# Optimization experiments

Hardware: AMD Instinct MI355X
Metric: run time of the kernel (lower is better)

Reference implementation:

```python
import jax, jax.numpy as jnp
import numpy as np

N, E, B = 25000, 400000, 64          # nodes, edges, graphs
F, ED, H, C = 32, 8, 4, 32           # feature/edge dims, heads, per-head dim
HC = H * C
L = 4                                # init conv + 3 stacked convs (same shapes)
LIN = 128


def setup_inputs() -> dict:
    key = jax.random.key(0)
    ks = jax.random.split(key, 24)
    s = 0.05
    inp = {
        "x": jax.random.normal(ks[0], (N, F), jnp.float32),
        "edge_attr": jax.random.normal(ks[1], (E, ED), jnp.float32),
        "edge_index": jax.random.randint(ks[2], (2, E), 0, N),
        "batch_index": jnp.sort(jax.random.randint(ks[3], (N,), 0, B)),
        # stacked TransformerConv params (leading dim = layer)
        "Wq": jax.random.normal(ks[4], (L, F, HC), jnp.float32) * s,
        "bq": jnp.zeros((L, HC), jnp.float32),
        "Wk": jax.random.normal(ks[5], (L, F, HC), jnp.float32) * s,
        "bk": jnp.zeros((L, HC), jnp.float32),
        "Wv": jax.random.normal(ks[6], (L, F, HC), jnp.float32) * s,
        "bv": jnp.zeros((L, HC), jnp.float32),
        "We": jax.random.normal(ks[7], (L, ED, HC), jnp.float32) * s,
        "be": jnp.zeros((L, HC), jnp.float32),
        "Wskip": jax.random.normal(ks[8], (L, F, HC), jnp.float32) * s,
        "bskip": jnp.zeros((L, HC), jnp.float32),
        "Wbeta": jax.random.normal(ks[9], (L, 3 * HC, 1), jnp.float32) * s,
        # per-layer Linear(H*C -> emb) + BatchNorm
        "Wlin": jax.random.normal(ks[10], (L, HC, F), jnp.float32) * s,
        "blin": jnp.zeros((L, F), jnp.float32),
        "bn_gamma": jnp.ones((L, F), jnp.float32),
        "bn_beta": jnp.zeros((L, F), jnp.float32),
        # readout MLP
        "W1": jax.random.normal(ks[11], (2 * F, LIN), jnp.float32) * s,
        "b1": jnp.zeros((LIN,), jnp.float32),
        "W2": jax.random.normal(ks[12], (LIN, LIN // 2), jnp.float32) * s,
        "b2": jnp.zeros((LIN // 2,), jnp.float32),
        "W3": jax.random.normal(ks[13], (LIN // 2, 1), jnp.float32) * s,
        "b3": jnp.zeros((1,), jnp.float32),
    }
    return inp


def _transformer_conv(x, edge_attr, src, dst, Wq, bq, Wk, bk, Wv, bv, We, be,
                      Wskip, bskip, Wbeta):
    """PyG TransformerConv(heads=H, concat=True, beta=True, edge_dim=ED), eval mode."""
    n = x.shape[0]
    q = (x @ Wq + bq).reshape(n, H, C)
    k = (x @ Wk + bk).reshape(n, H, C)
    v = (x @ Wv + bv).reshape(n, H, C)
    e = (edge_attr @ We + be).reshape(-1, H, C)          # [E,H,C]
    kj = k[src] + e                                       # key_j + edge
    alpha = jnp.einsum('ehc,ehc->eh', q[dst], kj) / np.sqrt(C).astype(np.float32)
    # segment softmax over incoming edges per destination node
    amax = jax.ops.segment_max(alpha, dst, num_segments=n)
    a = jnp.exp(alpha - amax[dst])
    denom = jax.ops.segment_sum(a, dst, num_segments=n)
    a = a / denom[dst]                                    # [E,H]
    msg = (v[src] + e) * a[:, :, None]
    out = jax.ops.segment_sum(msg, dst, num_segments=n).reshape(n, HC)
    x_skip = x @ Wskip + bskip
    beta = jax.nn.sigmoid(
        jnp.concatenate([out, x_skip, out - x_skip], axis=-1) @ Wbeta)  # [N,1]
    return beta * x_skip + (1.0 - beta) * out


def _bn(h, gamma, beta):
    m = h.mean(axis=0)
    v = h.var(axis=0)
    return (h - m) * jax.lax.rsqrt(v + 1e-5) * gamma + beta


def reference(x, edge_attr, edge_index, batch_index,
              Wq, bq, Wk, bk, Wv, bv, We, be, Wskip, bskip, Wbeta,
              Wlin, blin, bn_gamma, bn_beta, W1, b1, W2, b2, W3, b3):
    src, dst = edge_index[0], edge_index[1]
    counts = jax.ops.segment_sum(jnp.ones((N,), jnp.float32), batch_index,
                                 num_segments=B)[:, None]
    h = x
    rep = jnp.zeros((B, 2 * F), jnp.float32)
    for i in range(L):
        h = _transformer_conv(h, edge_attr, src, dst,
                              Wq[i], bq[i], Wk[i], bk[i], Wv[i], bv[i],
                              We[i], be[i], Wskip[i], bskip[i], Wbeta[i])
        h = jax.nn.elu(h @ Wlin[i] + blin[i])
        h = _bn(h, bn_gamma[i], bn_beta[i])
        if i > 0:  # original pools only inside the n_layers loop
            gmx = jax.ops.segment_max(h, batch_index, num_segments=B)
            gmean = jax.ops.segment_sum(h, batch_index, num_segments=B) / counts
            rep = rep + jnp.concatenate([gmx, gmean], axis=1)
    z = jax.nn.elu(rep @ W1 + b1)
    z = jax.nn.elu(z @ W2 + b2)
    return z @ W3 + b3  # [B,1]
```

## Files before the change

### kernel.cpp

```cpp
#include <hip/hip_runtime.h>
#include <hip/hip_bf16.h>
#include <hip/hip_fp16.h>
#include <math.h>

#define NN 25000
#define EE 400000
#define BB 64
#define FF 32
#define EDD 8
#define HH 4
#define CC 32
#define HCC 128
#define LL 4
#define LINN 128

#define RSQRT_C 0.17677669529663687f
#define NREP 16
#define LSTATS_WORDS (NREP * 64)


__global__ void deg_kernel(const int* __restrict__ dst, int* __restrict__ deg) {
    int i = blockIdx.x * blockDim.x + threadIdx.x;
    if (i < EE) atomicAdd(&deg[dst[i]], 1);
}

__global__ void gstart_kernel(const int* __restrict__ bidx, int* __restrict__ gstart) {
    int b = threadIdx.x;
    if (b <= BB) {
        int lo = 0, hi = NN;
        while (lo < hi) { int mid = (lo + hi) >> 1; if (bidx[mid] < b) lo = mid + 1; else hi = mid; }
        gstart[b] = lo;
    }
}

__global__ void scan1_kernel(const int* __restrict__ deg, int* __restrict__ rowp, int* __restrict__ blks) {
    __shared__ int s[256];
    int i = blockIdx.x * 256 + threadIdx.x;
    int v = (i < NN) ? deg[i] : 0;
    s[threadIdx.x] = v;
    __syncthreads();
    for (int off = 1; off < 256; off <<= 1) {
        int t = (threadIdx.x >= off) ? s[threadIdx.x - off] : 0;
        __syncthreads();
        s[threadIdx.x] += t;
        __syncthreads();
    }
    if (i < NN) rowp[i + 1] = s[threadIdx.x];
    if (threadIdx.x == 255) blks[blockIdx.x] = s[255];
    if (i == 0) rowp[0] = 0;
}

__global__ void scan2_kernel(int* __restrict__ blks, int nb) {
    __shared__ int s[128];
    int t = threadIdx.x;
    int v = (t < nb) ? blks[t] : 0;
    s[t] = v;
    __syncthreads();
    for (int off = 1; off < 128; off <<= 1) {
        int u = (t >= off) ? s[t - off] : 0;
        __syncthreads();
        s[t] += u;
        __syncthreads();
    }
    if (t < nb) blks[t] = s[t] - v;
}

__global__ void scan3_kernel(int* __restrict__ rowp, const int* __restrict__ blks) {
    int i = blockIdx.x * 256 + threadIdx.x;
    if (i < NN) rowp[i + 1] += blks[blockIdx.x];
}

__global__ void fill_kernel(const int* __restrict__ dst, const int* __restrict__ rowp,
                            int* __restrict__ cnt2, int* __restrict__ eid) {
    int i = blockIdx.x * blockDim.x + threadIdx.x;
    if (i < EE) {
        int d = dst[i];
        int pos = rowp[d] + atomicAdd(&cnt2[d], 1);
        eid[pos] = i;
    }
}

__global__ void sortseg_kernel(const int* __restrict__ rowp, int* __restrict__ eid) {
    int n = blockIdx.x * 256 + threadIdx.x;
    if (n >= NN) return;
    int b = rowp[n], e = rowp[n + 1];
    int d = e - b;
    if (d <= 1) return;
    if (d <= 64) {
        int buf[64];
        for (int i = 0; i < d; ++i) buf[i] = eid[b + i];
        for (int i = 1; i < d; ++i) {
            int key = buf[i];
            int j = i - 1;
            while (j >= 0 && buf[j] > key) { buf[j + 1] = buf[j]; --j; }
            buf[j + 1] = key;
        }
        for (int i = 0; i < d; ++i) eid[b + i] = buf[i];
    } else {
        for (int i = b + 1; i < e; ++i) {
            int key = eid[i];
            int j = i - 1;
            while (j >= b && eid[j] > key) { eid[j + 1] = eid[j]; --j; }
            eid[j + 1] = key;
        }
    }
}

__global__ void csr_gather_kernel(const int* __restrict__ csre, const int* __restrict__ srcA,
                                  const float* __restrict__ eattr,
                                  int* __restrict__ csrsrc, float4* __restrict__ ecsr) {
    int j = blockIdx.x * blockDim.x + threadIdx.x;
    if (j < EE) {
        int e = csre[j];
        csrsrc[j] = srcA[e];
        const float4* s = (const float4*)(eattr + (size_t)e * 8);
        ecsr[(size_t)j * 2] = s[0];
        ecsr[(size_t)j * 2 + 1] = s[1];
    }
}

__global__ __launch_bounds__(256) void qkvs_kernel(
    const float* __restrict__ hin,
    const float* __restrict__ Wq, const float* __restrict__ bq,
    const float* __restrict__ Wk, const float* __restrict__ bk,
    const float* __restrict__ Wv, const float* __restrict__ bv,
    const float* __restrict__ Ws, const float* __restrict__ bs,
    float2* __restrict__ qo,
    __half2* __restrict__ kvo,
    float2* __restrict__ so, float* __restrict__ lstats)
{
    if (blockIdx.x == 0) {
        for (int i = threadIdx.x; i < LSTATS_WORDS; i += 256) lstats[i] = 0.0f;
    }
    __shared__ float xs[32][32];
    int lane = threadIdx.x & 63;
    int sel = threadIdx.x >> 6;
    const float* W = (sel == 0) ? Wq : (sel == 1) ? Wk : (sel == 2) ? Wv : Ws;
    const float* bias = (sel == 0) ? bq : (sel == 1) ? bk : (sel == 2) ? bv : bs;
    float w0[32], w1[32];
#pragma unroll
    for (int f = 0; f < 32; ++f) {
        float2 t = *(const float2*)&W[f * 128 + 2 * lane];
        w0[f] = t.x; w1[f] = t.y;
    }
    float2 bvv = *(const float2*)&bias[2 * lane];

    int c = lane >> 1;
    int pr = lane & 1;
    int f2idx = c * 2 + pr;
    int h2k   = c * 4 + pr;
    int h2v   = c * 4 + 2 + pr;

    for (int chunk = blockIdx.x * 32; chunk < NN; chunk += gridDim.x * 32) {
        __syncthreads();
        for (int i = threadIdx.x; i < 1024; i += 256) {
            int nn = chunk + (i >> 5);
            xs[i >> 5][i & 31] = (nn < NN) ? hin[nn * 32 + (i & 31)] : 0.0f;
        }
        __syncthreads();
        int nmax = NN - chunk; if (nmax > 32) nmax = 32;
        for (int nl = 0; nl < nmax; ++nl) {
            float a0 = bvv.x, a1 = bvv.y;
#pragma unroll
            for (int f = 0; f < 32; ++f) {
                float xv = xs[nl][f];
                a0 += xv * w0[f];
                a1 += xv * w1[f];
            }
            size_t node = (size_t)(chunk + nl);
            if (sel == 0)      qo[node * 64 + f2idx] = make_float2(a0, a1);
            else if (sel == 1) kvo[node * 128 + h2k] = __float22half2_rn(make_float2(a0, a1));
            else if (sel == 2) kvo[node * 128 + h2v] = __float22half2_rn(make_float2(a0, a1));
            else               so[node * 64 + f2idx] = make_float2(a0, a1);
        }
    }
}

__global__ __launch_bounds__(256) void attn_kernel(
    const float4* __restrict__ qb4, const uint4* __restrict__ kvb4,
    const float4* __restrict__ skb4,
    const float4* __restrict__ eb4,
    const int* __restrict__ srcArr,
    const int* __restrict__ rowp,
    const float* __restrict__ WeL, const float* __restrict__ beL,
    const float* __restrict__ WbL,
    const float* __restrict__ WlinL, const float* __restrict__ blinL,
    float* __restrict__ hlin, float* __restrict__ bnpart)
{
    __shared__ __align__(16) float shc[4 * 128];
    __shared__ float sbn[64];

    int tid = threadIdx.x;
    if (tid < 64) sbn[tid] = 0.0f;
    __syncthreads();

    int w = tid >> 6;
    int lane = tid & 63;
    int n = blockIdx.x * 4 + w;

    if (n < NN) {
        int c = lane & 31;
        int h = lane >> 5;

        float4 q4 = qb4[(size_t)n * 32 + c];
        q4.x *= RSQRT_C; q4.y *= RSQRT_C; q4.z *= RSQRT_C; q4.w *= RSQRT_C;

        float r[8];
        float qbe;
        {
#pragma unroll
            for (int d = 0; d < 8; ++d) {
                float4 wd = *(const float4*)&WeL[d * 128 + 4 * c];
                r[d] = q4.x * wd.x + q4.y * wd.y + q4.z * wd.z + q4.w * wd.w;
            }
            float4 be4 = *(const float4*)&beL[4 * c];
            qbe = q4.x * be4.x + q4.y * be4.y + q4.z * be4.z + q4.w * be4.w;
#pragma unroll
            for (int off = 1; off <= 4; off <<= 1) {
#pragma unroll
                for (int d = 0; d < 8; ++d) r[d] += __shfl_xor(r[d], off);
                qbe += __shfl_xor(qbe, off);
            }
        }

        int beg = rowp[n], end = rowp[n + 1];
        int cnt = end - beg;
        int last = end - 1;

        float s = 0.0f, a0 = 0.0f, a1 = 0.0f, a2 = 0.0f, a3 = 0.0f;
        float t0 = 0.f, t1 = 0.f, t2 = 0.f, t3 = 0.f, t4 = 0.f, t5 = 0.f, t6 = 0.f, t7 = 0.f;

        uint4 kvA = make_uint4(0u, 0u, 0u, 0u), kvB = kvA;
        float4 eaA0 = make_float4(0.f, 0.f, 0.f, 0.f), eaA1 = eaA0;
        float4 eaB0 = eaA0, eaB1 = eaA0;
        int snC = 0, snD = 0;

        if (cnt > 0) {
            int j0 = beg + h;     j0 = (j0 < end) ? j0 : last;
            int j1 = beg + 2 + h; j1 = (j1 < end) ? j1 : last;
            int j2 = beg + 4 + h; j2 = (j2 < end) ? j2 : last;
            int j3 = beg + 6 + h; j3 = (j3 < end) ? j3 : last;
            int snA = srcArr[j0];
            int snB = srcArr[j1];
            snC = srcArr[j2];
            snD = srcArr[j3];
            kvA  = kvb4[(size_t)snA * 32 + c];
            kvB  = kvb4[(size_t)snB * 32 + c];
            eaA0 = eb4[(size_t)j0 * 2];
            eaA1 = eb4[(size_t)j0 * 2 + 1];
            eaB0 = eb4[(size_t)j1 * 2];
            eaB1 = eb4[(size_t)j1 * 2 + 1];
        }

        for (int jb = beg; jb < end; jb += 2) {
            int j = jb + h;
            uint4 kvC = kvb4[(size_t)snC * 32 + c];
            int jn = (j + 4 < end) ? j + 4 : last;
            float4 eaC0 = eb4[(size_t)jn * 2];
            float4 eaC1 = eb4[(size_t)jn * 2 + 1];
            int j8 = (j + 8 < end) ? j + 8 : last;
            int snE = srcArr[j8];

            float2 k01 = __half22float2(*(const __half2*)&kvA.x);
            float2 k23 = __half22float2(*(const __half2*)&kvA.y);
            float2 v01 = __half22float2(*(const __half2*)&kvA.z);
            float2 v23 = __half22float2(*(const __half2*)&kvA.w);

            float p = q4.x * k01.x + q4.y * k01.y + q4.z * k23.x + q4.w * k23.y;
            p += __shfl_xor(p, 1);
            p += __shfl_xor(p, 2);
            p += __shfl_xor(p, 4);
            float pe = eaA0.x * r[0] + eaA0.y * r[1] + eaA0.z * r[2] + eaA0.w * r[3]
                     + eaA1.x * r[4] + eaA1.y * r[5] + eaA1.z * r[6] + eaA1.w * r[7] + qbe;
            float wg = (j < end) ? __expf(p + pe) : 0.0f;
            s += wg;
            a0 = fmaf(wg, v01.x, a0);
            a1 = fmaf(wg, v01.y, a1);
            a2 = fmaf(wg, v23.x, a2);
            a3 = fmaf(wg, v23.y, a3);
            t0 = fmaf(wg, eaA0.x, t0);
            t1 = fmaf(wg, eaA0.y, t1);
            t2 = fmaf(wg, eaA0.z, t2);
            t3 = fmaf(wg, eaA0.w, t3);
            t4 = fmaf(wg, eaA1.x, t4);
            t5 = fmaf(wg, eaA1.y, t5);
            t6 = fmaf(wg, eaA1.z, t6);
            t7 = fmaf(wg, eaA1.w, t7);

            kvA = kvB; kvB = kvC;
            eaA0 = eaB0; eaA1 = eaB1; eaB0 = eaC0; eaB1 = eaC1;
            snC = snD; snD = snE;
        }

        s  += __shfl_xor(s, 32);
        a0 += __shfl_xor(a0, 32);
        a1 += __shfl_xor(a1, 32);
        a2 += __shfl_xor(a2, 32);
        a3 += __shfl_xor(a3, 32);
        t0 += __shfl_xor(t0, 32);
        t1 += __shfl_xor(t1, 32);
        t2 += __shfl_xor(t2, 32);
        t3 += __shfl_xor(t3, 32);
        t4 += __shfl_xor(t4, 32);
        t5 += __shfl_xor(t5, 32);
        t6 += __shfl_xor(t6, 32);
        t7 += __shfl_xor(t7, 32);

        {
            float4 wd;
            wd = *(const float4*)&WeL[0 * 128 + 4 * c];
            a0 = fmaf(t0, wd.x, a0); a1 = fmaf(t0, wd.y, a1); a2 = fmaf(t0, wd.z, a2); a3 = fmaf(t0, wd.w, a3);
            wd = *(const float4*)&WeL[1 * 128 + 4 * c];
            a0 = fmaf(t1, wd.x, a0); a1 = fmaf(t1, wd.y, a1); a2 = fmaf(t1, wd.z, a2); a3 = fmaf(t1, wd.w, a3);
            wd = *(const float4*)&WeL[2 * 128 + 4 * c];
            a0 = fmaf(t2, wd.x, a0); a1 = fmaf(t2, wd.y, a1); a2 = fmaf(t2, wd.z, a2); a3 = fmaf(t2, wd.w, a3);
            wd = *(const float4*)&WeL[3 * 128 + 4 * c];
            a0 = fmaf(t3, wd.x, a0); a1 = fmaf(t3, wd.y, a1); a2 = fmaf(t3, wd.z, a2); a3 = fmaf(t3, wd.w, a3);
            wd = *(const float4*)&WeL[4 * 128 + 4 * c];
            a0 = fmaf(t4, wd.x, a0); a1 = fmaf(t4, wd.y, a1); a2 = fmaf(t4, wd.z, a2); a3 = fmaf(t4, wd.w, a3);
            wd = *(const float4*)&WeL[5 * 128 + 4 * c];
            a0 = fmaf(t5, wd.x, a0); a1 = fmaf(t5, wd.y, a1); a2 = fmaf(t5, wd.z, a2); a3 = fmaf(t5, wd.w, a3);
            wd = *(const float4*)&WeL[6 * 128 + 4 * c];
            a0 = fmaf(t6, wd.x, a0); a1 = fmaf(t6, wd.y, a1); a2 = fmaf(t6, wd.z, a2); a3 = fmaf(t6, wd.w, a3);
            wd = *(const float4*)&WeL[7 * 128 + 4 * c];
            a0 = fmaf(t7, wd.x, a0); a1 = fmaf(t7, wd.y, a1); a2 = fmaf(t7, wd.z, a2); a3 = fmaf(t7, wd.w, a3);
            float4 be4 = *(const float4*)&beL[4 * c];
            a0 = fmaf(s, be4.x, a0);
            a1 = fmaf(s, be4.y, a1);
            a2 = fmaf(s, be4.z, a2);
            a3 = fmaf(s, be4.w, a3);
        }

        float rs = (cnt > 0) ? (1.0f / s) : 0.0f;
        float o0 = a0 * rs, o1 = a1 * rs, o2 = a2 * rs, o3 = a3 * rs;

        float4 sk4 = skb4[(size_t)n * 32 + c];
        float4 wbo = *(const float4*)&WbL[4 * c];
        float4 wbs = *(const float4*)&WbL[128 + 4 * c];
        float4 wbd = *(const float4*)&WbL[256 + 4 * c];

        float t = o0 * wbo.x + sk4.x * wbs.x + (o0 - sk4.x) * wbd.x
                + o1 * wbo.y + sk4.y * wbs.y + (o1 - sk4.y) * wbd.y
                + o2 * wbo.z + sk4.z * wbs.z + (o2 - sk4.z) * wbd.z
                + o3 * wbo.w + sk4.w * wbs.w + (o3 - sk4.w) * wbd.w;
#pragma unroll
        for (int off = 1; off <= 16; off <<= 1) t += __shfl_xor(t, off);
        float beta = 1.0f / (1.0f + __expf(-t));
        float4 hc4;
        hc4.x = beta * sk4.x + (1.0f - beta) * o0;
        hc4.y = beta * sk4.y + (1.0f - beta) * o1;
        hc4.z = beta * sk4.z + (1.0f - beta) * o2;
        hc4.w = beta * sk4.w + (1.0f - beta) * o3;
        if (h == 0) ((float4*)shc)[w * 32 + c] = hc4;
        int cc = lane & 31;
        int half = lane >> 5;
        float acc = 0.0f;
#pragma unroll 8
        for (int i = 0; i < 64; ++i) {
            int ch = half * 64 + i;
            acc += shc[w * 128 + ch] * WlinL[ch * 32 + cc];
        }
        acc += __shfl_xor(acc, 32);
        if (lane < 32) {
            float hv = acc + blinL[lane];
            hv = (hv > 0.0f) ? hv : expm1f(hv);
            hlin[n * 32 + lane] = hv;
            atomicAdd(&sbn[lane], hv);
            atomicAdd(&sbn[32 + lane], hv * hv);
        }
    }
    __syncthreads();
    if (tid < 64) atomicAdd(&bnpart[(blockIdx.x & (NREP - 1)) * 64 + tid], sbn[tid]);
}

__global__ __launch_bounds__(256) void bnpool_kernel(
    const float* __restrict__ hlin, const float* __restrict__ bnpart,
    const float* __restrict__ gamma, const float* __restrict__ bnbeta,
    const int* __restrict__ gstart,
    float* __restrict__ hc, float* __restrict__ rep, int doPool)
{
    __shared__ float sscale[32], sshift[32];
    __shared__ float smax[8][32], ssum[8][32];
    int tid = threadIdx.x;
    int ch = tid & 31, row = tid >> 5;
    if (tid < 32) {
        float sm = 0.0f, sq = 0.0f;
#pragma unroll
        for (int r = 0; r < NREP; ++r) { sm += bnpart[r * 64 + tid]; sq += bnpart[r * 64 + 32 + tid]; }
        float mean = sm * (1.0f / NN);
        float var = sq * (1.0f / NN) - mean * mean;
        float scale = gamma[tid] * rsqrtf(var + 1e-5f);
        sscale[tid] = scale;
        sshift[tid] = bnbeta[tid] - mean * scale;
    }
    __syncthreads();
    int g = blockIdx.x;
    int gs = gstart[g], ge = gstart[g + 1];
    float scale = sscale[ch], shift = sshift[ch];
    float mx = -1e30f, sum = 0.0f;
    for (int n = gs + row; n < ge; n += 8) {
        float val = hlin[n * 32 + ch] * scale + shift;
        hc[n * 32 + ch] = val;
        mx = fmaxf(mx, val);
        sum += val;
    }
    if (doPool) {
        smax[row][ch] = mx; ssum[row][ch] = sum;
        __syncthreads();
        if (row == 0) {
#pragma unroll
            for (int r = 1; r < 8; ++r) { mx = fmaxf(mx, smax[r][ch]); sum += ssum[r][ch]; }
            int cntg = ge - gs;
            if (cntg > 0) {
                rep[g * 64 + ch]      += mx;
                rep[g * 64 + 32 + ch] += sum / (float)cntg;
            }
        }
    }
}

__device__ __forceinline__ float eluf(float x) { return x > 0.0f ? x : expm1f(x); }

__global__ __launch_bounds__(128) void readout_kernel(
    const float* __restrict__ rep,
    const float* __restrict__ W1, const float* __restrict__ b1,
    const float* __restrict__ W2, const float* __restrict__ b2,
    const float* __restrict__ W3, const float* __restrict__ b3,
    float* __restrict__ out)
{
    __shared__ float sr[64];
    __shared__ float sz1[128];
    __shared__ float sz2[64];
    int g = blockIdx.x;
    int t = threadIdx.x;
    if (t < 64) sr[t] = rep[g * 64 + t];
    __syncthreads();
    float acc = b1[t];
#pragma unroll 8
    for (int i = 0; i < 64; ++i) acc += sr[i] * W1[i * 128 + t];
    sz1[t] = eluf(acc);
    __syncthreads();
    if (t < 64) {
        float a2 = b2[t];
#pragma unroll 8
        for (int i = 0; i < 128; ++i) a2 += sz1[i] * W2[i * 64 + t];
        sz2[t] = eluf(a2);
    }
    __syncthreads();
    if (t < 64) {
        float p = sz2[t] * W3[t];
#pragma unroll
        for (int off = 1; off <= 32; off <<= 1) p += __shfl_xor(p, off);
        if (t == 0) out[g] = p + b3[0];
    }
}


extern "C" void kernel_launch(void* const* d_in, const int* in_sizes, int n_in,
                              void* d_out, int out_size, void* d_ws, size_t ws_size,
                              hipStream_t stream) {
    const float* x      = (const float*)d_in[0];
    const float* eattr  = (const float*)d_in[1];
    const int*   eidx   = (const int*)d_in[2];
    const int*   bidx   = (const int*)d_in[3];
    const float* Wq     = (const float*)d_in[4];
    const float* bq     = (const float*)d_in[5];
    const float* Wk     = (const float*)d_in[6];
    const float* bk     = (const float*)d_in[7];
    const float* Wv     = (const float*)d_in[8];
    const float* bv     = (const float*)d_in[9];
    const float* We     = (const float*)d_in[10];
    const float* be     = (const float*)d_in[11];
    const float* Wskip  = (const float*)d_in[12];
    const float* bskip  = (const float*)d_in[13];
    const float* Wbeta  = (const float*)d_in[14];
    const float* Wlin   = (const float*)d_in[15];
    const float* blin   = (const float*)d_in[16];
    const float* bng    = (const float*)d_in[17];
    const float* bnb    = (const float*)d_in[18];
    const float* W1     = (const float*)d_in[19];
    const float* b1     = (const float*)d_in[20];
    const float* W2     = (const float*)d_in[21];
    const float* b2     = (const float*)d_in[22];
    const float* W3     = (const float*)d_in[23];
    const float* b3     = (const float*)d_in[24];
    float* out = (float*)d_out;

    char* ws = (char*)d_ws;
    size_t off = 0;
    auto alloc = [&](size_t bytes) -> char* {
        char* p = ws + off;
        off = (off + bytes + 255) & ~(size_t)255;
        return p;
    };
    int*    rowp   = (int*)alloc((NN + 1) * 4);
    int*    degcnt = (int*)alloc(2 * NN * 4);
    int*    deg    = degcnt;
    int*    cnt2   = degcnt + NN;
    int*    csre   = (int*)alloc(EE * 4);
    int*    blks   = (int*)alloc(128 * 4);
    int*    gstart = (int*)alloc((BB + 1) * 4);
    float*  rep    = (float*)alloc(BB * 64 * 4);
    float4* qB     = (float4*)alloc((size_t)NN * 32 * 16);
    uint4*  kvB    = (uint4*)alloc((size_t)NN * 32 * 16);
    float4* skB    = (float4*)alloc((size_t)NN * 32 * 16);
    float*  hlin   = (float*)alloc((size_t)NN * 32 * 4);
    float*  hcur   = (float*)alloc((size_t)NN * 32 * 4);
    float*  bnpart = (float*)alloc(LSTATS_WORDS * 4);
    int*    csrsrc = (int*)alloc(EE * 4);
    float4* ecsr   = (float4*)alloc((size_t)EE * 32);

    const int* srcA = eidx;
    const int* dstA = eidx + EE;

    (void)hipMemsetAsync(degcnt, 0, 2 * NN * 4, stream);
    (void)hipMemsetAsync(rep, 0, BB * 64 * 4, stream);

    deg_kernel<<<(EE + 255) / 256, 256, 0, stream>>>(dstA, deg);
    gstart_kernel<<<1, 128, 0, stream>>>(bidx, gstart);
    scan1_kernel<<<98, 256, 0, stream>>>(deg, rowp, blks);
    scan2_kernel<<<1, 128, 0, stream>>>(blks, 98);
    scan3_kernel<<<98, 256, 0, stream>>>(rowp, blks);
    fill_kernel<<<(EE + 255) / 256, 256, 0, stream>>>(dstA, rowp, cnt2, csre);
    sortseg_kernel<<<98, 256, 0, stream>>>(rowp, csre);
    csr_gather_kernel<<<(EE + 255) / 256, 256, 0, stream>>>(csre, srcA, eattr, csrsrc, ecsr);

    const float* hin = x;
    for (int l = 0; l < LL; ++l) {
        qkvs_kernel<<<782, 256, 0, stream>>>(
            hin,
            Wq + l * FF * HCC, bq + l * HCC,
            Wk + l * FF * HCC, bk + l * HCC,
            Wv + l * FF * HCC, bv + l * HCC,
            Wskip + l * FF * HCC, bskip + l * HCC,
            (float2*)qB, (__half2*)kvB, (float2*)skB, bnpart);

        attn_kernel<<<(NN + 3) / 4, 256, 0, stream>>>(
            qB, kvB, skB, ecsr, csrsrc, rowp,
            We + l * EDD * HCC, be + l * HCC,
            Wbeta + l * 3 * HCC,
            Wlin + l * HCC * FF, blin + l * FF,
            hlin, bnpart);

        bnpool_kernel<<<BB, 256, 0, stream>>>(hlin, bnpart, bng + l * FF, bnb + l * FF,
                                              gstart, hcur, rep, (l > 0) ? 1 : 0);
        hin = hcur;
    }

    readout_kernel<<<64, 128, 0, stream>>>(rep, W1, b1, W2, b2, W3, b3, out);
}
```

Baseline: 590.0 us.

## Split K/V into separate arrays and process four edges per wave

```diff
diff --git a/kernel.cpp b/kernel.cpp
--- a/kernel.cpp
+++ b/kernel.cpp
@@ -125,9 +125,9 @@
     const float* __restrict__ Wk, const float* __restrict__ bk,
     const float* __restrict__ Wv, const float* __restrict__ bv,
     const float* __restrict__ Ws, const float* __restrict__ bs,
-    float2* __restrict__ qo,
-    __half2* __restrict__ kvo,
-    float2* __restrict__ so, float* __restrict__ lstats)
+    float2* __restrict__ qo, __half2* __restrict__ ko,
+    __half2* __restrict__ vo, float2* __restrict__ so,
+    float* __restrict__ lstats)
 {
     if (blockIdx.x == 0) {
         for (int i = threadIdx.x; i < LSTATS_WORDS; i += 256) lstats[i] = 0.0f;
@@ -145,12 +145,6 @@
     }
     float2 bvv = *(const float2*)&bias[2 * lane];
 
-    int c = lane >> 1;
-    int pr = lane & 1;
-    int f2idx = c * 2 + pr;
-    int h2k   = c * 4 + pr;
-    int h2v   = c * 4 + 2 + pr;
-
     for (int chunk = blockIdx.x * 32; chunk < NN; chunk += gridDim.x * 32) {
         __syncthreads();
         for (int i = threadIdx.x; i < 1024; i += 256) {
@@ -168,17 +162,17 @@
                 a1 += xv * w1[f];
             }
             size_t node = (size_t)(chunk + nl);
-            if (sel == 0)      qo[node * 64 + f2idx] = make_float2(a0, a1);
-            else if (sel == 1) kvo[node * 128 + h2k] = __float22half2_rn(make_float2(a0, a1));
-            else if (sel == 2) kvo[node * 128 + h2v] = __float22half2_rn(make_float2(a0, a1));
-            else               so[node * 64 + f2idx] = make_float2(a0, a1);
+            if (sel == 0)      qo[node * 64 + lane] = make_float2(a0, a1);
+            else if (sel == 1) ko[node * 64 + lane] = __float22half2_rn(make_float2(a0, a1));
+            else if (sel == 2) vo[node * 64 + lane] = __float22half2_rn(make_float2(a0, a1));
+            else               so[node * 64 + lane] = make_float2(a0, a1);
         }
     }
 }
 
 __global__ __launch_bounds__(256) void attn_kernel(
-    const float4* __restrict__ qb4, const uint4* __restrict__ kvb4,
-    const float4* __restrict__ skb4,
+    const float4* __restrict__ qb4, const uint4* __restrict__ kb4,
+    const uint4* __restrict__ vb4, const float4* __restrict__ skb4,
     const float4* __restrict__ eb4,
     const int* __restrict__ srcArr,
     const int* __restrict__ rowp,
@@ -199,24 +193,30 @@
     int n = blockIdx.x * 4 + w;
 
     if (n < NN) {
-        int c = lane & 31;
-        int h = lane >> 5;
-
-        float4 q4 = qb4[(size_t)n * 32 + c];
-        q4.x *= RSQRT_C; q4.y *= RSQRT_C; q4.z *= RSQRT_C; q4.w *= RSQRT_C;
+        int cl = lane & 15;
+        int qt = lane >> 4;
+
+        const float4* qp = qb4 + (size_t)n * 32 + cl * 2;
+        float4 qa = qp[0], qb = qp[1];
+        qa.x *= RSQRT_C; qa.y *= RSQRT_C; qa.z *= RSQRT_C; qa.w *= RSQRT_C;
+        qb.x *= RSQRT_C; qb.y *= RSQRT_C; qb.z *= RSQRT_C; qb.w *= RSQRT_C;
 
         float r[8];
         float qbe;
         {
 #pragma unroll
             for (int d = 0; d < 8; ++d) {
-                float4 wd = *(const float4*)&WeL[d * 128 + 4 * c];
-                r[d] = q4.x * wd.x + q4.y * wd.y + q4.z * wd.z + q4.w * wd.w;
+                float4 wa = *(const float4*)&WeL[d * 128 + 8 * cl];
+                float4 wb = *(const float4*)&WeL[d * 128 + 8 * cl + 4];
+                r[d] = qa.x * wa.x + qa.y * wa.y + qa.z * wa.z + qa.w * wa.w
+                     + qb.x * wb.x + qb.y * wb.y + qb.z * wb.z + qb.w * wb.w;
             }
-            float4 be4 = *(const float4*)&beL[4 * c];
-            qbe = q4.x * be4.x + q4.y * be4.y + q4.z * be4.z + q4.w * be4.w;
-#pragma unroll
-            for (int off = 1; off <= 4; off <<= 1) {
+            float4 bea = *(const float4*)&beL[8 * cl];
+            float4 beb = *(const float4*)&beL[8 * cl + 4];
+            qbe = qa.x * bea.x + qa.y * bea.y + qa.z * bea.z + qa.w * bea.w
+                + qb.x * beb.x + qb.y * beb.y + qb.z * beb.z + qb.w * beb.w;
+#pragma unroll
+            for (int off = 1; off <= 2; off <<= 1) {
 #pragma unroll
                 for (int d = 0; d < 8; ++d) r[d] += __shfl_xor(r[d], off);
                 qbe += __shfl_xor(qbe, off);
@@ -227,57 +227,69 @@
         int cnt = end - beg;
         int last = end - 1;
 
-        float s = 0.0f, a0 = 0.0f, a1 = 0.0f, a2 = 0.0f, a3 = 0.0f;
+        float s = 0.0f;
+        float a0 = 0.f, a1 = 0.f, a2 = 0.f, a3 = 0.f, a4 = 0.f, a5 = 0.f, a6 = 0.f, a7 = 0.f;
         float t0 = 0.f, t1 = 0.f, t2 = 0.f, t3 = 0.f, t4 = 0.f, t5 = 0.f, t6 = 0.f, t7 = 0.f;
 
-        uint4 kvA = make_uint4(0u, 0u, 0u, 0u), kvB = kvA;
-        float4 eaA0 = make_float4(0.f, 0.f, 0.f, 0.f), eaA1 = eaA0;
-        float4 eaB0 = eaA0, eaB1 = eaA0;
+        uint4 kA = make_uint4(0u,0u,0u,0u), vA = kA, kB = kA, vB = kA;
+        float4 eaA0 = make_float4(0.f,0.f,0.f,0.f), eaA1 = eaA0, eaB0 = eaA0, eaB1 = eaA0;
         int snC = 0, snD = 0;
 
         if (cnt > 0) {
-            int j0 = beg + h;     j0 = (j0 < end) ? j0 : last;
-            int j1 = beg + 2 + h; j1 = (j1 < end) ? j1 : last;
-            int j2 = beg + 4 + h; j2 = (j2 < end) ? j2 : last;
-            int j3 = beg + 6 + h; j3 = (j3 < end) ? j3 : last;
+            int j0 = beg + qt;      j0 = (j0 < end) ? j0 : last;
+            int j1 = beg + 4 + qt;  j1 = (j1 < end) ? j1 : last;
+            int j2 = beg + 8 + qt;  j2 = (j2 < end) ? j2 : last;
+            int j3 = beg + 12 + qt; j3 = (j3 < end) ? j3 : last;
             int snA = srcArr[j0];
             int snB = srcArr[j1];
             snC = srcArr[j2];
             snD = srcArr[j3];
-            kvA  = kvb4[(size_t)snA * 32 + c];
-            kvB  = kvb4[(size_t)snB * 32 + c];
+            kA = kb4[(size_t)snA * 16 + cl];
+            vA = vb4[(size_t)snA * 16 + cl];
+            kB = kb4[(size_t)snB * 16 + cl];
+            vB = vb4[(size_t)snB * 16 + cl];
             eaA0 = eb4[(size_t)j0 * 2];
             eaA1 = eb4[(size_t)j0 * 2 + 1];
             eaB0 = eb4[(size_t)j1 * 2];
             eaB1 = eb4[(size_t)j1 * 2 + 1];
         }
 
-        for (int jb = beg; jb < end; jb += 2) {
-            int j = jb + h;
-            uint4 kvC = kvb4[(size_t)snC * 32 + c];
-            int jn = (j + 4 < end) ? j + 4 : last;
+        for (int jb = beg; jb < end; jb += 4) {
+            int j = jb + qt;
+            uint4 kC = kb4[(size_t)snC * 16 + cl];
+            uint4 vC = vb4[(size_t)snC * 16 + cl];
+            int jn = (j + 8 < end) ? j + 8 : last;
             float4 eaC0 = eb4[(size_t)jn * 2];
             float4 eaC1 = eb4[(size_t)jn * 2 + 1];
-            int j8 = (j + 8 < end) ? j + 8 : last;
-            int snE = srcArr[j8];
-
-            float2 k01 = __half22float2(*(const __half2*)&kvA.x);
-            float2 k23 = __half22float2(*(const __half2*)&kvA.y);
-            float2 v01 = __half22float2(*(const __half2*)&kvA.z);
-            float2 v23 = __half22float2(*(const __half2*)&kvA.w);
-
-            float p = q4.x * k01.x + q4.y * k01.y + q4.z * k23.x + q4.w * k23.y;
+            int j16 = (j + 16 < end) ? j + 16 : last;
+            int snE = srcArr[j16];
+
+            float2 k01 = __half22float2(*(const __half2*)&kA.x);
+            float2 k23 = __half22float2(*(const __half2*)&kA.y);
+            float2 k45 = __half22float2(*(const __half2*)&kA.z);
+            float2 k67 = __half22float2(*(const __half2*)&kA.w);
+
+            float p = qa.x * k01.x + qa.y * k01.y + qa.z * k23.x + qa.w * k23.y
+                    + qb.x * k45.x + qb.y * k45.y + qb.z * k67.x + qb.w * k67.y;
             p += __shfl_xor(p, 1);
             p += __shfl_xor(p, 2);
-            p += __shfl_xor(p, 4);
             float pe = eaA0.x * r[0] + eaA0.y * r[1] + eaA0.z * r[2] + eaA0.w * r[3]
                      + eaA1.x * r[4] + eaA1.y * r[5] + eaA1.z * r[6] + eaA1.w * r[7] + qbe;
             float wg = (j < end) ? __expf(p + pe) : 0.0f;
             s += wg;
+
+            float2 v01 = __half22float2(*(const __half2*)&vA.x);
+            float2 v23 = __half22float2(*(const __half2*)&vA.y);
+            float2 v45 = __half22float2(*(const __half2*)&vA.z);
+            float2 v67 = __half22float2(*(const __half2*)&vA.w);
             a0 = fmaf(wg, v01.x, a0);
             a1 = fmaf(wg, v01.y, a1);
             a2 = fmaf(wg, v23.x, a2);
             a3 = fmaf(wg, v23.y, a3);
+            a4 = fmaf(wg, v45.x, a4);
+            a5 = fmaf(wg, v45.y, a5);
+            a6 = fmaf(wg, v67.x, a6);
+            a7 = fmaf(wg, v67.y, a7);
             t0 = fmaf(wg, eaA0.x, t0);
             t1 = fmaf(wg, eaA0.y, t1);
             t2 = fmaf(wg, eaA0.z, t2);
@@ -287,71 +299,81 @@
             t6 = fmaf(wg, eaA1.z, t6);
             t7 = fmaf(wg, eaA1.w, t7);
 
-            kvA = kvB; kvB = kvC;
+            kA = kB; vA = vB; kB = kC; vB = vC;
             eaA0 = eaB0; eaA1 = eaB1; eaB0 = eaC0; eaB1 = eaC1;
             snC = snD; snD = snE;
         }
 
-        s  += __shfl_xor(s, 32);
-        a0 += __shfl_xor(a0, 32);
-        a1 += __shfl_xor(a1, 32);
-        a2 += __shfl_xor(a2, 32);
-        a3 += __shfl_xor(a3, 32);
-        t0 += __shfl_xor(t0, 32);
-        t1 += __shfl_xor(t1, 32);
-        t2 += __shfl_xor(t2, 32);
-        t3 += __shfl_xor(t3, 32);
-        t4 += __shfl_xor(t4, 32);
-        t5 += __shfl_xor(t5, 32);
-        t6 += __shfl_xor(t6, 32);
-        t7 += __shfl_xor(t7, 32);
+#pragma unroll
+        for (int off = 16; off <= 32; off <<= 1) {
+            s  += __shfl_xor(s, off);
+            a0 += __shfl_xor(a0, off); a1 += __shfl_xor(a1, off);
+            a2 += __shfl_xor(a2, off); a3 += __shfl_xor(a3, off);
+            a4 += __shfl_xor(a4, off); a5 += __shfl_xor(a5, off);
+            a6 += __shfl_xor(a6, off); a7 += __shfl_xor(a7, off);
+            t0 += __shfl_xor(t0, off); t1 += __shfl_xor(t1, off);
+            t2 += __shfl_xor(t2, off); t3 += __shfl_xor(t3, off);
+            t4 += __shfl_xor(t4, off); t5 += __shfl_xor(t5, off);
+            t6 += __shfl_xor(t6, off); t7 += __shfl_xor(t7, off);
+        }
 
         {
-            float4 wd;
-            wd = *(const float4*)&WeL[0 * 128 + 4 * c];
-            a0 = fmaf(t0, wd.x, a0); a1 = fmaf(t0, wd.y, a1); a2 = fmaf(t0, wd.z, a2); a3 = fmaf(t0, wd.w, a3);
-            wd = *(const float4*)&WeL[1 * 128 + 4 * c];
-            a0 = fmaf(t1, wd.x, a0); a1 = fmaf(t1, wd.y, a1); a2 = fmaf(t1, wd.z, a2); a3 = fmaf(t1, wd.w, a3);
-            wd = *(const float4*)&WeL[2 * 128 + 4 * c];
-            a0 = fmaf(t2, wd.x, a0); a1 = fmaf(t2, wd.y, a1); a2 = fmaf(t2, wd.z, a2); a3 = fmaf(t2, wd.w, a3);
-            wd = *(const float4*)&WeL[3 * 128 + 4 * c];
-            a0 = fmaf(t3, wd.x, a0); a1 = fmaf(t3, wd.y, a1); a2 = fmaf(t3, wd.z, a2); a3 = fmaf(t3, wd.w, a3);
-            wd = *(const float4*)&WeL[4 * 128 + 4 * c];
-            a0 = fmaf(t4, wd.x, a0); a1 = fmaf(t4, wd.y, a1); a2 = fmaf(t4, wd.z, a2); a3 = fmaf(t4, wd.w, a3);
-            wd = *(const float4*)&WeL[5 * 128 + 4 * c];
-            a0 = fmaf(t5, wd.x, a0); a1 = fmaf(t5, wd.y, a1); a2 = fmaf(t5, wd.z, a2); a3 = fmaf(t5, wd.w, a3);
-            wd = *(const float4*)&WeL[6 * 128 + 4 * c];
-            a0 = fmaf(t6, wd.x, a0); a1 = fmaf(t6, wd.y, a1); a2 = fmaf(t6, wd.z, a2); a3 = fmaf(t6, wd.w, a3);
-            wd = *(const float4*)&WeL[7 * 128 + 4 * c];
-            a0 = fmaf(t7, wd.x, a0); a1 = fmaf(t7, wd.y, a1); a2 = fmaf(t7, wd.z, a2); a3 = fmaf(t7, wd.w, a3);
-            float4 be4 = *(const float4*)&beL[4 * c];
-            a0 = fmaf(s, be4.x, a0);
-            a1 = fmaf(s, be4.y, a1);
-            a2 = fmaf(s, be4.z, a2);
-            a3 = fmaf(s, be4.w, a3);
+            float td[8] = { t0, t1, t2, t3, t4, t5, t6, t7 };
+#pragma unroll
+            for (int d = 0; d < 8; ++d) {
+                float4 wa = *(const float4*)&WeL[d * 128 + 8 * cl];
+                float4 wb = *(const float4*)&WeL[d * 128 + 8 * cl + 4];
+                a0 = fmaf(td[d], wa.x, a0); a1 = fmaf(td[d], wa.y, a1);
+                a2 = fmaf(td[d], wa.z, a2); a3 = fmaf(td[d], wa.w, a3);
+                a4 = fmaf(td[d], wb.x, a4); a5 = fmaf(td[d], wb.y, a5);
+                a6 = fmaf(td[d], wb.z, a6); a7 = fmaf(td[d], wb.w, a7);
+            }
+            float4 bea = *(const float4*)&beL[8 * cl];
+            float4 beb = *(const float4*)&beL[8 * cl + 4];
+            a0 = fmaf(s, bea.x, a0); a1 = fmaf(s, bea.y, a1);
+            a2 = fmaf(s, bea.z, a2); a3 = fmaf(s, bea.w, a3);
+            a4 = fmaf(s, beb.x, a4); a5 = fmaf(s, beb.y, a5);
+            a6 = fmaf(s, beb.z, a6); a7 = fmaf(s, beb.w, a7);
         }
 
         float rs = (cnt > 0) ? (1.0f / s) : 0.0f;
         float o0 = a0 * rs, o1 = a1 * rs, o2 = a2 * rs, o3 = a3 * rs;
-
-        float4 sk4 = skb4[(size_t)n * 32 + c];
-        float4 wbo = *(const float4*)&WbL[4 * c];
-        float4 wbs = *(const float4*)&WbL[128 + 4 * c];
-        float4 wbd = *(const float4*)&WbL[256 + 4 * c];
-
-        float t = o0 * wbo.x + sk4.x * wbs.x + (o0 - sk4.x) * wbd.x
-                + o1 * wbo.y + sk4.y * wbs.y + (o1 - sk4.y) * wbd.y
-                + o2 * wbo.z + sk4.z * wbs.z + (o2 - sk4.z) * wbd.z
-                + o3 * wbo.w + sk4.w * wbs.w + (o3 - sk4.w) * wbd.w;
-#pragma unroll
-        for (int off = 1; off <= 16; off <<= 1) t += __shfl_xor(t, off);
-        float beta = 1.0f / (1.0f + __expf(-t));
-        float4 hc4;
-        hc4.x = beta * sk4.x + (1.0f - beta) * o0;
-        hc4.y = beta * sk4.y + (1.0f - beta) * o1;
-        hc4.z = beta * sk4.z + (1.0f - beta) * o2;
-        hc4.w = beta * sk4.w + (1.0f - beta) * o3;
-        if (h == 0) ((float4*)shc)[w * 32 + c] = hc4;
+        float o4 = a4 * rs, o5 = a5 * rs, o6 = a6 * rs, o7 = a7 * rs;
+
+        const float4* skp = skb4 + (size_t)n * 32 + cl * 2;
+        float4 ska = skp[0], skb_ = skp[1];
+        float4 woa = *(const float4*)&WbL[8 * cl];
+        float4 wob = *(const float4*)&WbL[8 * cl + 4];
+        float4 wsa = *(const float4*)&WbL[128 + 8 * cl];
+        float4 wsb = *(const float4*)&WbL[128 + 8 * cl + 4];
+        float4 wda = *(const float4*)&WbL[256 + 8 * cl];
+        float4 wdb = *(const float4*)&WbL[256 + 8 * cl + 4];
+
+        float tt = o0 * woa.x + ska.x * wsa.x + (o0 - ska.x) * wda.x
+                 + o1 * woa.y + ska.y * wsa.y + (o1 - ska.y) * wda.y
+                 + o2 * woa.z + ska.z * wsa.z + (o2 - ska.z) * wda.z
+                 + o3 * woa.w + ska.w * wsa.w + (o3 - ska.w) * wda.w
+                 + o4 * wob.x + skb_.x * wsb.x + (o4 - skb_.x) * wdb.x
+                 + o5 * wob.y + skb_.y * wsb.y + (o5 - skb_.y) * wdb.y
+                 + o6 * wob.z + skb_.z * wsb.z + (o6 - skb_.z) * wdb.z
+                 + o7 * wob.w + skb_.w * wsb.w + (o7 - skb_.w) * wdb.w;
+#pragma unroll
+        for (int off = 1; off <= 8; off <<= 1) tt += __shfl_xor(tt, off);
+        float beta = 1.0f / (1.0f + __expf(-tt));
+        float om = 1.0f - beta;
+        if (qt == 0) {
+            float4 hca, hcb;
+            hca.x = beta * ska.x + om * o0;
+            hca.y = beta * ska.y + om * o1;
+            hca.z = beta * ska.z + om * o2;
+            hca.w = beta * ska.w + om * o3;
+            hcb.x = beta * skb_.x + om * o4;
+            hcb.y = beta * skb_.y + om * o5;
+            hcb.z = beta * skb_.z + om * o6;
+            hcb.w = beta * skb_.w + om * o7;
+            ((float4*)shc)[w * 32 + cl * 2]     = hca;
+            ((float4*)shc)[w * 32 + cl * 2 + 1] = hcb;
+        }
         int cc = lane & 31;
         int half = lane >> 5;
         float acc = 0.0f;
@@ -502,7 +524,8 @@
     int*    gstart = (int*)alloc((BB + 1) * 4);
     float*  rep    = (float*)alloc(BB * 64 * 4);
     float4* qB     = (float4*)alloc((size_t)NN * 32 * 16);
-    uint4*  kvB    = (uint4*)alloc((size_t)NN * 32 * 16);
+    uint4*  kB     = (uint4*)alloc((size_t)NN * 16 * 16);
+    uint4*  vB     = (uint4*)alloc((size_t)NN * 16 * 16);
     float4* skB    = (float4*)alloc((size_t)NN * 32 * 16);
     float*  hlin   = (float*)alloc((size_t)NN * 32 * 4);
     float*  hcur   = (float*)alloc((size_t)NN * 32 * 4);
@@ -533,10 +556,10 @@
             Wk + l * FF * HCC, bk + l * HCC,
             Wv + l * FF * HCC, bv + l * HCC,
             Wskip + l * FF * HCC, bskip + l * HCC,
-            (float2*)qB, (__half2*)kvB, (float2*)skB, bnpart);
+            (float2*)qB, (__half2*)kB, (__half2*)vB, (float2*)skB, bnpart);
 
         attn_kernel<<<(NN + 3) / 4, 256, 0, stream>>>(
-            qB, kvB, skB, ecsr, csrsrc, rowp,
+            qB, kB, vB, skB, ecsr, csrsrc, rowp,
             We + l * EDD * HCC, be + l * HCC,
             Wbeta + l * 3 * HCC,
             Wlin + l * HCC * FF, blin + l * FF,
```

New measurement: 595.8 us. No clear change (+1.0%).
